# Kernel optimization log

Hardware: AMD Instinct MI355X
Metric: run time of the kernel (lower is better)

## Reference

```python
import jax, jax.numpy as jnp
import numpy as np
import math

N, L, C, H = 16, 2048, 512, 8
D = C // H  # head channels = 64


def setup_inputs() -> dict:
    key = jax.random.key(0)
    ks = jax.random.split(key, 18)
    s = 1.0 / math.sqrt(C)
    sd = 1.0 / math.sqrt(D)
    return {
        "x_q": jax.random.normal(ks[0], (N, L, C), jnp.float32),
        "x_kv": jax.random.normal(ks[1], (N, L, C), jnp.float32),
        "Wq": jax.random.normal(ks[2], (C, C), jnp.float32) * s,
        "bq": jax.random.normal(ks[3], (C,), jnp.float32) * s,
        "wqa": jax.random.normal(ks[4], (D,), jnp.float32) * sd,
        "bqa": jax.random.normal(ks[5], (1,), jnp.float32) * sd,
        "Wk": jax.random.normal(ks[6], (C, C), jnp.float32) * s,
        "bk": jax.random.normal(ks[7], (C,), jnp.float32) * s,
        "wka": jax.random.normal(ks[8], (D,), jnp.float32) * sd,
        "bka": jax.random.normal(ks[9], (1,), jnp.float32) * sd,
        "Wv": jax.random.normal(ks[10], (C, C), jnp.float32) * s,
        "bv": jax.random.normal(ks[11], (C,), jnp.float32) * s,
        "Wt": jax.random.normal(ks[12], (D, D), jnp.float32) * sd,
        "bt": jax.random.normal(ks[13], (D,), jnp.float32) * sd,
        "Wp": jax.random.normal(ks[14], (C, C), jnp.float32) * s,
        "bp": jax.random.normal(ks[15], (C,), jnp.float32) * s,
    }


def _separate_heads(x):
    # (N, L, C) -> (N, H, L, D)
    n, l, _ = x.shape
    return x.reshape(n, l, H, D).transpose(0, 2, 1, 3)


def reference(x_q, x_kv, Wq, bq, wqa, bqa, Wk, bk, wka, bka, Wv, bv, Wt, bt, Wp, bp):
    inv_sqrt_d = 1.0 / math.sqrt(D)

    # Query projection (torch Linear: y = x @ W.T + b), dropout is identity (eval)
    q = _separate_heads(x_q @ Wq.T + bq)  # (N,H,L,D)
    # Additive pooling of queries over L
    q_score = (jnp.einsum("nhld,d->nhl", q, wqa) + bqa[0]) * inv_sqrt_d
    q_weight = jax.nn.softmax(q_score, axis=-1)  # (N,H,L)
    pooled_q = jnp.einsum("nhl,nhld->nhd", q_weight, q)[:, :, None, :]  # (N,H,1,D)

    # Key projection, gated by pooled query
    k = _separate_heads(x_kv @ Wk.T + bk)  # (N,H,L,D)
    kq = k * pooled_q
    k_score = (jnp.einsum("nhld,d->nhl", kq, wka) + bka[0]) * inv_sqrt_d
    k_weight = jax.nn.softmax(k_score, axis=-1)
    pooled_k = jnp.einsum("nhl,nhld->nhd", k_weight, k)[:, :, None, :]  # (N,H,1,D)

    # Value projection, gated by pooled key, then per-head transform
    v = _separate_heads(x_kv @ Wv.T + bv)  # (N,H,L,D)
    kv = jnp.einsum("nhld,ed->nhle", v * pooled_k, Wt) + bt

    out = kv + q  # (N,H,L,D)
    out = out.transpose(0, 2, 1, 3).reshape(out.shape[0], out.shape[2], C)  # group heads
    return out @ Wp.T + bp
```

## Files before the change

kernel.cpp:

```cpp
#include <hip/hip_runtime.h>
#include <hip/hip_bf16.h>
#include <math.h>

#define NB 16
#define LL 2048
#define CC 512
#define HH 8
#define MM (NB*LL)

typedef __attribute__((ext_vector_type(8))) short bf16x8;
typedef __attribute__((ext_vector_type(4))) float f32x4;
typedef __attribute__((ext_vector_type(8))) unsigned short u16x8;

__device__ inline unsigned short f2bf(float x) {
    __hip_bfloat16 b = __float2bfloat16(x);
    return __builtin_bit_cast(unsigned short, b);
}
__device__ inline float bf2f(unsigned short u) {
    __hip_bfloat16 b = __builtin_bit_cast(__hip_bfloat16, u);
    return __bfloat162float(b);
}
__device__ inline void split2(float x, unsigned short& h, unsigned short& l) {
    unsigned short hh = f2bf(x);
    float fh = bf2f(hh);
    h = hh;
    l = f2bf(x - fh);
}

__global__ __launch_bounds__(256)
void prep_kernel(const float* __restrict__ Wq, const float* __restrict__ Wk,
                 const float* __restrict__ Wv, const float* __restrict__ Wt,
                 const float* __restrict__ bt, const float* __restrict__ Wp,
                 const float* __restrict__ bp,
                 unsigned short* __restrict__ Bqh, unsigned short* __restrict__ Bql,
                 unsigned short* __restrict__ Bkh, unsigned short* __restrict__ Bkl,
                 unsigned short* __restrict__ Bvh, unsigned short* __restrict__ Bvl,
                 unsigned short* __restrict__ WBh, unsigned short* __restrict__ WBl,
                 float* __restrict__ cvec)
{
    const int t = blockIdx.x * 256 + threadIdx.x;
    const int c = t >> 10;
    const int k = t & 1023;
    float val;
    if (k < 512) {
        const int h = k >> 6, d = k & 63;
        float s = 0.f;
        #pragma unroll 8
        for (int e = 0; e < 64; ++e) s += Wt[e * 64 + d] * Wp[c * CC + h * 64 + e];
        val = s;
    } else {
        val = Wp[c * CC + (k - 512)];
    }
    unsigned short hh, ll;
    split2(val, hh, ll);
    const size_t pw = (((size_t)(k >> 3) * 512) + c) * 8 + (k & 7);
    WBh[pw] = hh; WBl[pw] = ll;
    if (k < 512) {
        split2(Wq[c * CC + k], hh, ll); Bqh[pw] = hh; Bql[pw] = ll;
        split2(Wk[c * CC + k], hh, ll); Bkh[pw] = hh; Bkl[pw] = ll;
        split2(Wv[c * CC + k], hh, ll); Bvh[pw] = hh; Bvl[pw] = ll;
    }
    if (k == 0) {
        float cv = bp[c];
        for (int j = 0; j < 512; ++j) cv += bt[j & 63] * Wp[c * CC + j];
        cvec[c] = cv;
    }
}

template<int KT1, int KT2, bool G1>
__global__ __launch_bounds__(512, 4)
void gemm_f32a(const float* __restrict__ A1, const float* __restrict__ A2,
               const float* __restrict__ gate,
               const unsigned short* __restrict__ Bh, const unsigned short* __restrict__ Bl,
               const float* __restrict__ bias, float* __restrict__ out)
{
    constexpr int KT = KT1 + KT2;
    __shared__ __align__(16) unsigned short sAh[4096], sAl[4096];
    __shared__ __align__(16) unsigned short sBh[8192], sBl[8192];
    const int tid = threadIdx.x;
    const int flat = blockIdx.x;
    const int xcd = flat & 7, idx = flat >> 3;
    const int mt = xcd * 32 + (idx >> 1);
    const int nt = idx & 1;
    const int n0 = nt * 256, m0 = mt * 128;
    const int l = tid & 63, w = tid >> 6;
    const int wm = w >> 2, wn = w & 3;
    const int smp = mt >> 4;

    const int arow = tid & 127, akp = tid >> 7;
    const int bcol = tid & 255, bkp0 = tid >> 8;

    f32x4 acc[4][4] = {};

    float4 pa0, pa1;
    uint4 pbh0, pbh1, pbl0, pbl1;

    auto loadTile = [&](int kt) {
        const float* Asrc; int k0g; bool g;
        if (KT2 == 0 || kt < KT1) { Asrc = A1; k0g = kt * 32; g = G1; }
        else                      { Asrc = A2; k0g = (kt - KT1) * 32; g = false; }
        const float* p = Asrc + (size_t)(m0 + arow) * CC + k0g + akp * 8;
        float4 a0 = *(const float4*)p, a1 = *(const float4*)(p + 4);
        if (g) {
            const float* gp = gate + smp * CC + k0g + akp * 8;
            const float4 g0 = *(const float4*)gp, g1 = *(const float4*)(gp + 4);
            a0.x *= g0.x; a0.y *= g0.y; a0.z *= g0.z; a0.w *= g0.w;
            a1.x *= g1.x; a1.y *= g1.y; a1.z *= g1.z; a1.w *= g1.w;
        }
        pa0 = a0; pa1 = a1;
        const int kpg = kt * 4;
        const size_t ob0 = (((size_t)(kpg + bkp0) * 512) + n0 + bcol) * 8;
        const size_t ob1 = (((size_t)(kpg + bkp0 + 2) * 512) + n0 + bcol) * 8;
        pbh0 = *(const uint4*)&Bh[ob0]; pbh1 = *(const uint4*)&Bh[ob1];
        pbl0 = *(const uint4*)&Bl[ob0]; pbl1 = *(const uint4*)&Bl[ob1];
    };

    auto storeTile = [&]() {
        float x[8];
        *(float4*)&x[0] = pa0; *(float4*)&x[4] = pa1;
        u16x8 hv, lv;
        #pragma unroll
        for (int j = 0; j < 8; ++j) { unsigned short h, lo; split2(x[j], h, lo); hv[j] = h; lv[j] = lo; }
        *(u16x8*)&sAh[(akp * 128 + arow) * 8] = hv;
        *(u16x8*)&sAl[(akp * 128 + arow) * 8] = lv;
        *(uint4*)&sBh[(bkp0 * 256 + bcol) * 8] = pbh0;
        *(uint4*)&sBh[((bkp0 + 2) * 256 + bcol) * 8] = pbh1;
        *(uint4*)&sBl[(bkp0 * 256 + bcol) * 8] = pbl0;
        *(uint4*)&sBl[((bkp0 + 2) * 256 + bcol) * 8] = pbl1;
    };

    loadTile(0);

    for (int kt = 0; kt < KT; ++kt) {
        __syncthreads();
        storeTile();
        __syncthreads();
        if (kt + 1 < KT) loadTile(kt + 1);

        const int g = l >> 4;
        const int rA = wm * 64 + (l & 15);
        const int rB = wn * 64 + (l & 15);
        const bf16x8* vAh = (const bf16x8*)sAh; const bf16x8* vAl = (const bf16x8*)sAl;
        const bf16x8* vBh = (const bf16x8*)sBh; const bf16x8* vBl = (const bf16x8*)sBl;
        bf16x8 ah[4], al[4], bh[4], bl[4];
        #pragma unroll
        for (int f = 0; f < 4; ++f) {
            ah[f] = vAh[g * 128 + rA + f * 16];
            al[f] = vAl[g * 128 + rA + f * 16];
            bh[f] = vBh[g * 256 + rB + f * 16];
            bl[f] = vBl[g * 256 + rB + f * 16];
        }
        #pragma unroll
        for (int i = 0; i < 4; ++i)
            #pragma unroll
            for (int j = 0; j < 4; ++j) {
                acc[i][j] = __builtin_amdgcn_mfma_f32_16x16x32_bf16(ah[i], bh[j], acc[i][j], 0, 0, 0);
                acc[i][j] = __builtin_amdgcn_mfma_f32_16x16x32_bf16(ah[i], bl[j], acc[i][j], 0, 0, 0);
                acc[i][j] = __builtin_amdgcn_mfma_f32_16x16x32_bf16(al[i], bh[j], acc[i][j], 0, 0, 0);
            }
    }

    const int rowb = (l >> 4) * 4, colb = l & 15;
    #pragma unroll
    for (int j = 0; j < 4; ++j) {
        const int c = n0 + wn * 64 + j * 16 + colb;
        const float bv = bias[c];
        #pragma unroll
        for (int i = 0; i < 4; ++i) {
            const int r = m0 + wm * 64 + i * 16 + rowb;
            #pragma unroll
            for (int e = 0; e < 4; ++e)
                out[(size_t)(r + e) * CC + c] = acc[i][j][e] + bv;
        }
    }
}

__global__ __launch_bounds__(256)
void pool_stage1(const float* __restrict__ src, const float* __restrict__ wvec,
                 const float* __restrict__ bscal, float* __restrict__ partials,
                 int modeK)
{
    __shared__ float sm[256];
    __shared__ float se[4];
    const int nh = blockIdx.x, chunk = blockIdx.y;
    const int n = nh >> 3, h = nh & 7;
    const int tid = threadIdx.x;
    const int wave = tid >> 6, d = tid & 63;
    const float wv = modeK ? wvec[nh * 64 + d] : wvec[d];
    const float b = bscal[0];
    const float* base = src + (size_t)n * LL * CC + h * 64;
    float accv = 0.f, acce = 0.f;
    const int l0 = chunk * 128 + wave;
    #pragma unroll 4
    for (int it = 0; it < 32; ++it) {
        const int ll = l0 + it * 4;
        const float x = base[(size_t)ll * CC + d];
        float s = x * wv;
        s += __shfl_xor(s, 1, 64);
        s += __shfl_xor(s, 2, 64);
        s += __shfl_xor(s, 4, 64);
        s += __shfl_xor(s, 8, 64);
        s += __shfl_xor(s, 16, 64);
        s += __shfl_xor(s, 32, 64);
        const float e = expf((s + b) * 0.125f);
        accv += e * x;
        acce += e;
    }
    sm[tid] = accv;
    if (d == 0) se[wave] = acce;
    __syncthreads();
    if (wave == 0) {
        const float pv = sm[d] + sm[64 + d] + sm[128 + d] + sm[192 + d];
        float* pr = partials + ((size_t)nh * 16 + chunk) * 65;
        pr[d] = pv;
        if (d == 0) pr[64] = se[0] + se[1] + se[2] + se[3];
    }
}

__global__ __launch_bounds__(64)
void pool_stage2(const float* __restrict__ partials, const float* __restrict__ postmul,
                 float* __restrict__ pooled)
{
    const int nh = blockIdx.x, d = threadIdx.x;
    float pv = 0.f, pe = 0.f;
    #pragma unroll
    for (int c = 0; c < 16; ++c) {
        const float* pr = partials + ((size_t)nh * 16 + c) * 65;
        pv += pr[d];
        pe += pr[64];
    }
    float p = pv / pe;
    if (postmul) p *= postmul[d];
    pooled[nh * 64 + d] = p;
}

#define OFF_BQH   0ull
#define OFF_BQL   524288ull
#define OFF_BKH   1048576ull
#define OFF_BKL   1572864ull
#define OFF_BVH   2097152ull
#define OFF_BVL   2621440ull
#define OFF_WBH   3145728ull
#define OFF_WBL   4194304ull
#define OFF_CVEC  5242880ull
#define OFF_GQ    5259264ull
#define OFF_PK    5292032ull
#define OFF_PART  5324800ull
#define OFF_QBUF  8388608ull
#define OFF_KV    75497472ull

extern "C" void kernel_launch(void* const* d_in, const int* in_sizes, int n_in,
                              void* d_out, int out_size, void* d_ws, size_t ws_size,
                              hipStream_t stream) {
    const float* x_q  = (const float*)d_in[0];
    const float* x_kv = (const float*)d_in[1];
    const float* Wq   = (const float*)d_in[2];
    const float* bq   = (const float*)d_in[3];
    const float* wqa  = (const float*)d_in[4];
    const float* bqa  = (const float*)d_in[5];
    const float* Wk   = (const float*)d_in[6];
    const float* bk   = (const float*)d_in[7];
    const float* wka  = (const float*)d_in[8];
    const float* bka  = (const float*)d_in[9];
    const float* Wv   = (const float*)d_in[10];
    const float* bv   = (const float*)d_in[11];
    const float* Wt   = (const float*)d_in[12];
    const float* bt   = (const float*)d_in[13];
    const float* Wp   = (const float*)d_in[14];
    const float* bp   = (const float*)d_in[15];
    float* out = (float*)d_out;
    char* ws = (char*)d_ws;

    unsigned short* Bqh = (unsigned short*)(ws + OFF_BQH);
    unsigned short* Bql = (unsigned short*)(ws + OFF_BQL);
    unsigned short* Bkh = (unsigned short*)(ws + OFF_BKH);
    unsigned short* Bkl = (unsigned short*)(ws + OFF_BKL);
    unsigned short* Bvh = (unsigned short*)(ws + OFF_BVH);
    unsigned short* Bvl = (unsigned short*)(ws + OFF_BVL);
    unsigned short* WBh = (unsigned short*)(ws + OFF_WBH);
    unsigned short* WBl = (unsigned short*)(ws + OFF_WBL);
    float* cvec = (float*)(ws + OFF_CVEC);
    float* gq   = (float*)(ws + OFF_GQ);
    float* pk   = (float*)(ws + OFF_PK);
    float* part = (float*)(ws + OFF_PART);
    float* qbuf  = (float*)(ws + OFF_QBUF);
    float* kvbuf = (float*)(ws + OFF_KV);

    const dim3 pgrid(NB * HH, 16);

    prep_kernel<<<2048, 256, 0, stream>>>(Wq, Wk, Wv, Wt, bt, Wp, bp,
                                          Bqh, Bql, Bkh, Bkl, Bvh, Bvl, WBh, WBl, cvec);
    gemm_f32a<16, 0, false><<<512, 512, 0, stream>>>(x_q, nullptr, nullptr, Bqh, Bql, bq, qbuf);
    pool_stage1<<<pgrid, 256, 0, stream>>>(qbuf, wqa, bqa, part, 0);
    pool_stage2<<<NB * HH, 64, 0, stream>>>(part, wka, gq);
    gemm_f32a<16, 0, false><<<512, 512, 0, stream>>>(x_kv, nullptr, nullptr, Bkh, Bkl, bk, kvbuf);
    pool_stage1<<<pgrid, 256, 0, stream>>>(kvbuf, gq, bka, part, 1);
    pool_stage2<<<NB * HH, 64, 0, stream>>>(part, nullptr, pk);
    gemm_f32a<16, 0, false><<<512, 512, 0, stream>>>(x_kv, nullptr, nullptr, Bvh, Bvl, bv, kvbuf);
    gemm_f32a<16, 16, true><<<512, 512, 0, stream>>>(kvbuf, qbuf, pk, WBh, WBl, cvec, out);
}
```

Before: 517.3 us.

## Store projections as pre-split bf16 packed layout, merge Q/K GEMMs, fold gate into weights

Projection GEMMs now write their outputs already split into hi/lo bf16 in the k-packed layout, staged through shared memory. The final GEMM can then load A tiles directly without a per-tile fp32 split or gate multiply. The Q and K projections are merged into one launch of 1024 blocks. The pooled-key gate is folded into per-sample copies of the combined Wt·Wp weight by a new gate_wb kernel. The cost is extra workspace, a larger per-sample B matrix read in the final GEMM, and a more complex epilogue with extra barriers.

```diff
diff --git a/kernel.cpp b/kernel.cpp
--- a/kernel.cpp
+++ b/kernel.cpp
@@ -35,30 +35,28 @@
                  unsigned short* __restrict__ Bqh, unsigned short* __restrict__ Bql,
                  unsigned short* __restrict__ Bkh, unsigned short* __restrict__ Bkl,
                  unsigned short* __restrict__ Bvh, unsigned short* __restrict__ Bvl,
-                 unsigned short* __restrict__ WBh, unsigned short* __restrict__ WBl,
-                 float* __restrict__ cvec)
+                 unsigned short* __restrict__ WPTh, unsigned short* __restrict__ WPTl,
+                 float* __restrict__ WBFP, float* __restrict__ cvec)
 {
     const int t = blockIdx.x * 256 + threadIdx.x;
     const int c = t >> 10;
     const int k = t & 1023;
-    float val;
+    unsigned short hh, ll;
     if (k < 512) {
         const int h = k >> 6, d = k & 63;
         float s = 0.f;
         #pragma unroll 8
         for (int e = 0; e < 64; ++e) s += Wt[e * 64 + d] * Wp[c * CC + h * 64 + e];
-        val = s;
+        const size_t pq = (((size_t)(k >> 3) * 512) + c) * 8 + (k & 7);
+        WBFP[pq] = s;
+        split2(Wq[c * CC + k], hh, ll); Bqh[pq] = hh; Bql[pq] = ll;
+        split2(Wk[c * CC + k], hh, ll); Bkh[pq] = hh; Bkl[pq] = ll;
+        split2(Wv[c * CC + k], hh, ll); Bvh[pq] = hh; Bvl[pq] = ll;
     } else {
-        val = Wp[c * CC + (k - 512)];
-    }
-    unsigned short hh, ll;
-    split2(val, hh, ll);
-    const size_t pw = (((size_t)(k >> 3) * 512) + c) * 8 + (k & 7);
-    WBh[pw] = hh; WBl[pw] = ll;
-    if (k < 512) {
-        split2(Wq[c * CC + k], hh, ll); Bqh[pw] = hh; Bql[pw] = ll;
-        split2(Wk[c * CC + k], hh, ll); Bkh[pw] = hh; Bkl[pw] = ll;
-        split2(Wv[c * CC + k], hh, ll); Bvh[pw] = hh; Bvl[pw] = ll;
+        const int kl = k - 512;
+        const size_t pw = (((size_t)(kl >> 3) * 512) + c) * 8 + (kl & 7);
+        split2(Wp[c * CC + kl], hh, ll);
+        WPTh[pw] = hh; WPTl[pw] = ll;
     }
     if (k == 0) {
         float cv = bp[c];
@@ -67,16 +65,178 @@
     }
 }
 
-template<int KT1, int KT2, bool G1>
+__global__ __launch_bounds__(256)
+void gate_wb(const float* __restrict__ WBFP, const float* __restrict__ pk,
+             unsigned short* __restrict__ WBGh, unsigned short* __restrict__ WBGl)
+{
+    const int u = blockIdx.x * 256 + threadIdx.x;
+    const int smp = u >> 15;
+    const int r = u & 32767;
+    const int kp = r >> 9, c = r & 511;
+    const float* w = &WBFP[(((size_t)kp * 512) + c) * 8];
+    const float* p = &pk[smp * 512 + kp * 8];
+    u16x8 hv, lv;
+    #pragma unroll
+    for (int j = 0; j < 8; ++j) {
+        unsigned short h, lo;
+        split2(w[j] * p[j], h, lo);
+        hv[j] = h; lv[j] = lo;
+    }
+    const size_t o = (((size_t)smp * 64 + kp) * 512 + c) * 8;
+    *(u16x8*)&WBGh[o] = hv;
+    *(u16x8*)&WBGl[o] = lv;
+}
+
 __global__ __launch_bounds__(512, 4)
-void gemm_f32a(const float* __restrict__ A1, const float* __restrict__ A2,
-               const float* __restrict__ gate,
-               const unsigned short* __restrict__ Bh, const unsigned short* __restrict__ Bl,
-               const float* __restrict__ bias, float* __restrict__ out)
-{
-    constexpr int KT = KT1 + KT2;
-    __shared__ __align__(16) unsigned short sAh[4096], sAl[4096];
-    __shared__ __align__(16) unsigned short sBh[8192], sBl[8192];
+void gemm_proj(const float* __restrict__ A0, const float* __restrict__ A1,
+               const unsigned short* __restrict__ B0h, const unsigned short* __restrict__ B0l,
+               const unsigned short* __restrict__ B1h, const unsigned short* __restrict__ B1l,
+               const float* __restrict__ bias0, const float* __restrict__ bias1,
+               unsigned short* __restrict__ O0h, unsigned short* __restrict__ O0l,
+               unsigned short* __restrict__ O1h, unsigned short* __restrict__ O1l,
+               int ntl)
+{
+    __shared__ __align__(16) unsigned short smem[24576];
+    unsigned short* sAh = smem;
+    unsigned short* sAl = smem + 4096;
+    unsigned short* sBh = smem + 8192;
+    unsigned short* sBl = smem + 16384;
+
+    const int tid = threadIdx.x;
+    const int flat = blockIdx.x;
+    const int xcd = flat & 7, idx = flat >> 3;
+    const int mt = xcd * 32 + (idx >> ntl);
+    const int ntv = idx & ((1 << ntl) - 1);
+    const int type = ntv >> 1;
+    const int n0 = (ntv & 1) * 256;
+    const int m0 = mt * 128;
+    const int l = tid & 63, w = tid >> 6;
+    const int wm = w >> 2, wn = w & 3;
+
+    const float* Asrc = type ? A1 : A0;
+    const unsigned short* Bh = type ? B1h : B0h;
+    const unsigned short* Bl = type ? B1l : B0l;
+    const float* bias = type ? bias1 : bias0;
+    unsigned short* Oh = type ? O1h : O0h;
+    unsigned short* Ol = type ? O1l : O0l;
+
+    const int arow = tid & 127, akp = tid >> 7;
+    const int bcol = tid & 255, bkp0 = tid >> 8;
+
+    f32x4 acc[4][4] = {};
+
+    float4 pa0, pa1;
+    uint4 pbh0, pbh1, pbl0, pbl1;
+
+    auto loadTile = [&](int kt) {
+        const int k0 = kt * 32;
+        const float* p = Asrc + (size_t)(m0 + arow) * CC + k0 + akp * 8;
+        pa0 = *(const float4*)p; pa1 = *(const float4*)(p + 4);
+        const int kpg = kt * 4;
+        const size_t ob0 = (((size_t)(kpg + bkp0) * 512) + n0 + bcol) * 8;
+        const size_t ob1 = (((size_t)(kpg + bkp0 + 2) * 512) + n0 + bcol) * 8;
+        pbh0 = *(const uint4*)&Bh[ob0]; pbh1 = *(const uint4*)&Bh[ob1];
+        pbl0 = *(const uint4*)&Bl[ob0]; pbl1 = *(const uint4*)&Bl[ob1];
+    };
+
+    auto storeTile = [&]() {
+        float x[8];
+        *(float4*)&x[0] = pa0; *(float4*)&x[4] = pa1;
+        u16x8 hv, lv;
+        #pragma unroll
+        for (int j = 0; j < 8; ++j) { unsigned short h, lo; split2(x[j], h, lo); hv[j] = h; lv[j] = lo; }
+        *(u16x8*)&sAh[(akp * 128 + arow) * 8] = hv;
+        *(u16x8*)&sAl[(akp * 128 + arow) * 8] = lv;
+        *(uint4*)&sBh[(bkp0 * 256 + bcol) * 8] = pbh0;
+        *(uint4*)&sBh[((bkp0 + 2) * 256 + bcol) * 8] = pbh1;
+        *(uint4*)&sBl[(bkp0 * 256 + bcol) * 8] = pbl0;
+        *(uint4*)&sBl[((bkp0 + 2) * 256 + bcol) * 8] = pbl1;
+    };
+
+    loadTile(0);
+
+    for (int kt = 0; kt < 16; ++kt) {
+        __syncthreads();
+        storeTile();
+        __syncthreads();
+        if (kt + 1 < 16) loadTile(kt + 1);
+
+        const int g = l >> 4;
+        const int rA = wm * 64 + (l & 15);
+        const int rB = wn * 64 + (l & 15);
+        const bf16x8* vAh = (const bf16x8*)sAh; const bf16x8* vAl = (const bf16x8*)sAl;
+        const bf16x8* vBh = (const bf16x8*)sBh; const bf16x8* vBl = (const bf16x8*)sBl;
+        bf16x8 ah[4], al[4], bh[4], bl[4];
+        #pragma unroll
+        for (int f = 0; f < 4; ++f) {
+            ah[f] = vAh[g * 128 + rA + f * 16];
+            al[f] = vAl[g * 128 + rA + f * 16];
+            bh[f] = vBh[g * 256 + rB + f * 16];
+            bl[f] = vBl[g * 256 + rB + f * 16];
+        }
+        #pragma unroll
+        for (int i = 0; i < 4; ++i)
+            #pragma unroll
+            for (int j = 0; j < 4; ++j) {
+                acc[i][j] = __builtin_amdgcn_mfma_f32_16x16x32_bf16(ah[i], bh[j], acc[i][j], 0, 0, 0);
+                acc[i][j] = __builtin_amdgcn_mfma_f32_16x16x32_bf16(ah[i], bl[j], acc[i][j], 0, 0, 0);
+                acc[i][j] = __builtin_amdgcn_mfma_f32_16x16x32_bf16(al[i], bh[j], acc[i][j], 0, 0, 0);
+            }
+    }
+
+    const int rowb = (l >> 4) * 4, colb = l & 15;
+    const int hw = wn >> 1;
+    const int clbase = (wn & 1) * 64;
+    unsigned short* sP = smem;
+    for (int half = 0; half < 2; ++half) {
+        for (int part = 0; part < 2; ++part) {
+            __syncthreads();
+            if (hw == half) {
+                #pragma unroll
+                for (int j = 0; j < 4; ++j) {
+                    const float bv = bias[n0 + half * 128 + clbase + j * 16 + colb];
+                    #pragma unroll
+                    for (int i = 0; i < 4; ++i) {
+                        #pragma unroll
+                        for (int e = 0; e < 4; ++e) {
+                            const int row = wm * 64 + i * 16 + rowb + e;
+                            const int cl = clbase + j * 16 + colb;
+                            unsigned short h, lo;
+                            split2(acc[i][j][e] + bv, h, lo);
+                            sP[row * 132 + cl] = part ? lo : h;
+                        }
+                    }
+                }
+            }
+            __syncthreads();
+            unsigned short* OP = part ? Ol : Oh;
+            #pragma unroll
+            for (int pass = 0; pass < 4; ++pass) {
+                const int o = pass * 4 + (tid >> 7);
+                const int row = tid & 127;
+                const uint2 v0 = *(const uint2*)&sP[row * 132 + o * 8];
+                const uint2 v1 = *(const uint2*)&sP[row * 132 + o * 8 + 4];
+                const int cg = n0 + half * 128 + o * 8;
+                uint4 val; val.x = v0.x; val.y = v0.y; val.z = v1.x; val.w = v1.y;
+                *(uint4*)&OP[((size_t)(cg >> 3) * MM + m0 + row) * 8] = val;
+            }
+        }
+    }
+}
+
+__global__ __launch_bounds__(512, 4)
+void gemm_final(const unsigned short* __restrict__ VPh, const unsigned short* __restrict__ VPl,
+                const unsigned short* __restrict__ QPh, const unsigned short* __restrict__ QPl,
+                const unsigned short* __restrict__ WBGh, const unsigned short* __restrict__ WBGl,
+                const unsigned short* __restrict__ WPTh, const unsigned short* __restrict__ WPTl,
+                const float* __restrict__ cvec, float* __restrict__ out)
+{
+    __shared__ __align__(16) unsigned short smem[24576];
+    unsigned short* sAh = smem;
+    unsigned short* sAl = smem + 4096;
+    unsigned short* sBh = smem + 8192;
+    unsigned short* sBl = smem + 16384;
+
     const int tid = threadIdx.x;
     const int flat = blockIdx.x;
     const int xcd = flat & 7, idx = flat >> 3;
@@ -92,37 +252,29 @@
 
     f32x4 acc[4][4] = {};
 
-    float4 pa0, pa1;
-    uint4 pbh0, pbh1, pbl0, pbl1;
+    uint4 pah, pal, pbh0, pbh1, pbl0, pbl1;
 
     auto loadTile = [&](int kt) {
-        const float* Asrc; int k0g; bool g;
-        if (KT2 == 0 || kt < KT1) { Asrc = A1; k0g = kt * 32; g = G1; }
-        else                      { Asrc = A2; k0g = (kt - KT1) * 32; g = false; }
-        const float* p = Asrc + (size_t)(m0 + arow) * CC + k0g + akp * 8;
-        float4 a0 = *(const float4*)p, a1 = *(const float4*)(p + 4);
-        if (g) {
-            const float* gp = gate + smp * CC + k0g + akp * 8;
-            const float4 g0 = *(const float4*)gp, g1 = *(const float4*)(gp + 4);
-            a0.x *= g0.x; a0.y *= g0.y; a0.z *= g0.z; a0.w *= g0.w;
-            a1.x *= g1.x; a1.y *= g1.y; a1.z *= g1.z; a1.w *= g1.w;
-        }
-        pa0 = a0; pa1 = a1;
-        const int kpg = kt * 4;
-        const size_t ob0 = (((size_t)(kpg + bkp0) * 512) + n0 + bcol) * 8;
-        const size_t ob1 = (((size_t)(kpg + bkp0 + 2) * 512) + n0 + bcol) * 8;
-        pbh0 = *(const uint4*)&Bh[ob0]; pbh1 = *(const uint4*)&Bh[ob1];
-        pbl0 = *(const uint4*)&Bl[ob0]; pbl1 = *(const uint4*)&Bl[ob1];
+        const int ktl = kt & 15;
+        const unsigned short* Ah_ = (kt < 16) ? VPh : QPh;
+        const unsigned short* Al_ = (kt < 16) ? VPl : QPl;
+        const size_t ao = (((size_t)ktl * 4 + akp) * MM + m0 + arow) * 8;
+        pah = *(const uint4*)&Ah_[ao];
+        pal = *(const uint4*)&Al_[ao];
+        const unsigned short* Bh_;
+        const unsigned short* Bl_;
+        size_t bb;
+        if (kt < 16) { Bh_ = WBGh + (size_t)smp * 262144; Bl_ = WBGl + (size_t)smp * 262144; bb = kt * 4; }
+        else         { Bh_ = WPTh; Bl_ = WPTl; bb = (kt - 16) * 4; }
+        const size_t ob0 = ((bb + bkp0) * 512 + n0 + bcol) * 8;
+        const size_t ob1 = ((bb + bkp0 + 2) * 512 + n0 + bcol) * 8;
+        pbh0 = *(const uint4*)&Bh_[ob0]; pbh1 = *(const uint4*)&Bh_[ob1];
+        pbl0 = *(const uint4*)&Bl_[ob0]; pbl1 = *(const uint4*)&Bl_[ob1];
     };
 
     auto storeTile = [&]() {
-        float x[8];
-        *(float4*)&x[0] = pa0; *(float4*)&x[4] = pa1;
-        u16x8 hv, lv;
-        #pragma unroll
-        for (int j = 0; j < 8; ++j) { unsigned short h, lo; split2(x[j], h, lo); hv[j] = h; lv[j] = lo; }
-        *(u16x8*)&sAh[(akp * 128 + arow) * 8] = hv;
-        *(u16x8*)&sAl[(akp * 128 + arow) * 8] = lv;
+        *(uint4*)&sAh[(akp * 128 + arow) * 8] = pah;
+        *(uint4*)&sAl[(akp * 128 + arow) * 8] = pal;
         *(uint4*)&sBh[(bkp0 * 256 + bcol) * 8] = pbh0;
         *(uint4*)&sBh[((bkp0 + 2) * 256 + bcol) * 8] = pbh1;
         *(uint4*)&sBl[(bkp0 * 256 + bcol) * 8] = pbl0;
@@ -131,11 +283,11 @@
 
     loadTile(0);
 
-    for (int kt = 0; kt < KT; ++kt) {
+    for (int kt = 0; kt < 32; ++kt) {
         __syncthreads();
         storeTile();
         __syncthreads();
-        if (kt + 1 < KT) loadTile(kt + 1);
+        if (kt + 1 < 32) loadTile(kt + 1);
 
         const int g = l >> 4;
         const int rA = wm * 64 + (l & 15);
@@ -164,7 +316,7 @@
     #pragma unroll
     for (int j = 0; j < 4; ++j) {
         const int c = n0 + wn * 64 + j * 16 + colb;
-        const float bv = bias[c];
+        const float bv = cvec[c];
         #pragma unroll
         for (int i = 0; i < 4; ++i) {
             const int r = m0 + wm * 64 + i * 16 + rowb;
@@ -176,9 +328,9 @@
 }
 
 __global__ __launch_bounds__(256)
-void pool_stage1(const float* __restrict__ src, const float* __restrict__ wvec,
-                 const float* __restrict__ bscal, float* __restrict__ partials,
-                 int modeK)
+void pool_stage1(const unsigned short* __restrict__ Ph, const unsigned short* __restrict__ Pl,
+                 const float* __restrict__ wvec, const float* __restrict__ bscal,
+                 float* __restrict__ partials, int modeK)
 {
     __shared__ float sm[256];
     __shared__ float se[4];
@@ -188,13 +340,15 @@
     const int wave = tid >> 6, d = tid & 63;
     const float wv = modeK ? wvec[nh * 64 + d] : wvec[d];
     const float b = bscal[0];
-    const float* base = src + (size_t)n * LL * CC + h * 64;
+    const size_t rbase = ((size_t)(h * 8 + (d >> 3))) * MM + (size_t)n * LL;
+    const int kc = d & 7;
     float accv = 0.f, acce = 0.f;
     const int l0 = chunk * 128 + wave;
     #pragma unroll 4
     for (int it = 0; it < 32; ++it) {
         const int ll = l0 + it * 4;
-        const float x = base[(size_t)ll * CC + d];
+        const size_t a = (rbase + ll) * 8 + kc;
+        const float x = bf2f(Ph[a]) + bf2f(Pl[a]);
         float s = x * wv;
         s += __shfl_xor(s, 1, 64);
         s += __shfl_xor(s, 2, 64);
@@ -240,14 +394,19 @@
 #define OFF_BKL   1572864ull
 #define OFF_BVH   2097152ull
 #define OFF_BVL   2621440ull
-#define OFF_WBH   3145728ull
-#define OFF_WBL   4194304ull
+#define OFF_WPTH  3145728ull
+#define OFF_WPTL  3670016ull
+#define OFF_WBFP  4194304ull
 #define OFF_CVEC  5242880ull
-#define OFF_GQ    5259264ull
-#define OFF_PK    5292032ull
-#define OFF_PART  5324800ull
-#define OFF_QBUF  8388608ull
-#define OFF_KV    75497472ull
+#define OFF_GQ    5246976ull
+#define OFF_PK    5279744ull
+#define OFF_PART  5312512ull
+#define OFF_WBGH  6291456ull
+#define OFF_WBGL  14680064ull
+#define OFF_QPH   23068672ull
+#define OFF_QPL   56623104ull
+#define OFF_KPH   90177536ull
+#define OFF_KPL   123731968ull
 
 extern "C" void kernel_launch(void* const* d_in, const int* in_sizes, int n_in,
                               void* d_out, int out_size, void* d_ws, size_t ws_size,
@@ -271,31 +430,40 @@
     float* out = (float*)d_out;
     char* ws = (char*)d_ws;
 
-    unsigned short* Bqh = (unsigned short*)(ws + OFF_BQH);
-    unsigned short* Bql = (unsigned short*)(ws + OFF_BQL);
-    unsigned short* Bkh = (unsigned short*)(ws + OFF_BKH);
-    unsigned short* Bkl = (unsigned short*)(ws + OFF_BKL);
-    unsigned short* Bvh = (unsigned short*)(ws + OFF_BVH);
-    unsigned short* Bvl = (unsigned short*)(ws + OFF_BVL);
-    unsigned short* WBh = (unsigned short*)(ws + OFF_WBH);
-    unsigned short* WBl = (unsigned short*)(ws + OFF_WBL);
+    unsigned short* Bqh  = (unsigned short*)(ws + OFF_BQH);
+    unsigned short* Bql  = (unsigned short*)(ws + OFF_BQL);
+    unsigned short* Bkh  = (unsigned short*)(ws + OFF_BKH);
+    unsigned short* Bkl  = (unsigned short*)(ws + OFF_BKL);
+    unsigned short* Bvh  = (unsigned short*)(ws + OFF_BVH);
+    unsigned short* Bvl  = (unsigned short*)(ws + OFF_BVL);
+    unsigned short* WPTh = (unsigned short*)(ws + OFF_WPTH);
+    unsigned short* WPTl = (unsigned short*)(ws + OFF_WPTL);
+    float* WBFP = (float*)(ws + OFF_WBFP);
     float* cvec = (float*)(ws + OFF_CVEC);
     float* gq   = (float*)(ws + OFF_GQ);
     float* pk   = (float*)(ws + OFF_PK);
     float* part = (float*)(ws + OFF_PART);
-    float* qbuf  = (float*)(ws + OFF_QBUF);
-    float* kvbuf = (float*)(ws + OFF_KV);
+    unsigned short* WBGh = (unsigned short*)(ws + OFF_WBGH);
+    unsigned short* WBGl = (unsigned short*)(ws + OFF_WBGL);
+    unsigned short* QPh  = (unsigned short*)(ws + OFF_QPH);
+    unsigned short* QPl  = (unsigned short*)(ws + OFF_QPL);
+    unsigned short* KPh  = (unsigned short*)(ws + OFF_KPH);
+    unsigned short* KPl  = (unsigned short*)(ws + OFF_KPL);
 
     const dim3 pgrid(NB * HH, 16);
 
     prep_kernel<<<2048, 256, 0, stream>>>(Wq, Wk, Wv, Wt, bt, Wp, bp,
-                                          Bqh, Bql, Bkh, Bkl, Bvh, Bvl, WBh, WBl, cvec);
-    gemm_f32a<16, 0, false><<<512, 512, 0, stream>>>(x_q, nullptr, nullptr, Bqh, Bql, bq, qbuf);
-    pool_stage1<<<pgrid, 256, 0, stream>>>(qbuf, wqa, bqa, part, 0);
+                                          Bqh, Bql, Bkh, Bkl, Bvh, Bvl,
+                                          WPTh, WPTl, WBFP, cvec);
+    gemm_proj<<<1024, 512, 0, stream>>>(x_q, x_kv, Bqh, Bql, Bkh, Bkl, bq, bk,
+                                        QPh, QPl, KPh, KPl, 2);
+    pool_stage1<<<pgrid, 256, 0, stream>>>(QPh, QPl, wqa, bqa, part, 0);
     pool_stage2<<<NB * HH, 64, 0, stream>>>(part, wka, gq);
-    gemm_f32a<16, 0, false><<<512, 512, 0, stream>>>(x_kv, nullptr, nullptr, Bkh, Bkl, bk, kvbuf);
-    pool_stage1<<<pgrid, 256, 0, stream>>>(kvbuf, gq, bka, part, 1);
+    pool_stage1<<<pgrid, 256, 0, stream>>>(KPh, KPl, gq, bka, part, 1);
     pool_stage2<<<NB * HH, 64, 0, stream>>>(part, nullptr, pk);
-    gemm_f32a<16, 0, false><<<512, 512, 0, stream>>>(x_kv, nullptr, nullptr, Bvh, Bvl, bv, kvbuf);
-    gemm_f32a<16, 16, true><<<512, 512, 0, stream>>>(kvbuf, qbuf, pk, WBh, WBl, cvec, out);
-}
+    gate_wb<<<2048, 256, 0, stream>>>(WBFP, pk, WBGh, WBGl);
+    gemm_proj<<<512, 512, 0, stream>>>(x_kv, x_kv, Bvh, Bvl, Bvh, Bvl, bv, bv,
+                                       KPh, KPl, KPh, KPl, 1);
+    gemm_final<<<512, 512, 0, stream>>>(KPh, KPl, QPh, QPl, WBGh, WBGl,
+                                        WPTh, WPTl, cvec, out);
+}
```

New measurement: 487.4 us. 1.06x faster.
